# Optimization experiments

Measured on AMD Instinct MI355X. Metric: run time of the kernel, lower is better.

## Reference

```python
import jax, jax.numpy as jnp
import numpy as np
from jax import lax

PAD = 2          # shift_size // 2
SHIFT = 5        # shift_size


def _soft_shift(fp, gw, gb, axis):
    """fp: padded feature map [B,C,Hp,Wp]; gw: [S,C] 1x1-conv weight; gb: [S].
    Gated soft-shift along `axis` (2=H, 3=W), then crop padding."""
    logits = jnp.einsum('bchw,sc->bshw', fp, gw) + gb[None, :, None, None]
    w = jax.nn.softmax(logits, axis=1)  # [B,S,Hp,Wp]
    acc = jnp.zeros_like(fp)
    for i, s in enumerate(range(-PAD, PAD + 1)):
        acc = acc + jnp.roll(fp, s, axis=axis) * w[:, i:i + 1]
    return acc[:, :, PAD:-PAD, PAD:-PAD]


def _dwconv(x, w, b):
    # x: [B,C,H,W], w: [C,1,3,3] depthwise, b: [C]
    y = lax.conv_general_dilated(x, w, window_strides=(1, 1), padding='SAME',
                                 dimension_numbers=('NCHW', 'OIHW', 'NCHW'),
                                 feature_group_count=x.shape[1])
    return y + b[None, :, None, None]


def setup_inputs() -> dict:
    key = jax.random.key(0)
    ks = jax.random.split(key, 12)
    B, H, W = 16, 128, 128
    C, Ch = 96, 384
    x = jax.random.normal(ks[0], (B, H * W, C), dtype=jnp.float32)
    fc1_w = jax.random.normal(ks[1], (C, Ch), dtype=jnp.float32) * 0.02
    fc1_b = jnp.zeros((Ch,), dtype=jnp.float32)
    dw_w = jax.random.normal(ks[2], (Ch, 1, 3, 3), dtype=jnp.float32) * np.sqrt(2.0 / 9.0)
    dw_b = jnp.zeros((Ch,), dtype=jnp.float32)
    fc2_w = jax.random.normal(ks[3], (Ch, C), dtype=jnp.float32) * 0.02
    fc2_b = jnp.zeros((C,), dtype=jnp.float32)
    gh_w = jax.random.normal(ks[4], (SHIFT, C), dtype=jnp.float32) * np.sqrt(2.0 / SHIFT)
    gh_b = jnp.zeros((SHIFT,), dtype=jnp.float32)
    gw_w = jax.random.normal(ks[5], (SHIFT, Ch), dtype=jnp.float32) * np.sqrt(2.0 / SHIFT)
    gw_b = jnp.zeros((SHIFT,), dtype=jnp.float32)
    return {"x": x, "H": H, "W": W,
            "fc1_w": fc1_w, "fc1_b": fc1_b, "dw_w": dw_w, "dw_b": dw_b,
            "fc2_w": fc2_w, "fc2_b": fc2_b,
            "gh_w": gh_w, "gh_b": gh_b, "gw_w": gw_w, "gw_b": gw_b}


def reference(x, H, W, fc1_w, fc1_b, dw_w, dw_b, fc2_w, fc2_b, gh_w, gh_b, gw_w, gw_b):
    B, N, C = x.shape
    # soft-shift along H on input channels
    fmap = jnp.transpose(x, (0, 2, 1)).reshape(B, C, H, W)
    fmap_p = jnp.pad(fmap, ((0, 0), (0, 0), (PAD, PAD), (PAD, PAD)))
    mixed_h = _soft_shift(fmap_p, gh_w, gh_b, axis=2)          # [B,C,H,W]
    tokens = jnp.transpose(mixed_h.reshape(B, C, H * W), (0, 2, 1))
    tokens = tokens @ fc1_w + fc1_b                            # [B,N,Ch]
    Ch = tokens.shape[-1]
    t = jnp.transpose(tokens, (0, 2, 1)).reshape(B, Ch, H, W)
    t = _dwconv(t, dw_w, dw_b)
    tokens = jnp.transpose(t.reshape(B, Ch, H * W), (0, 2, 1))
    tokens = jax.nn.gelu(tokens, approximate=False)
    # soft-shift along W on hidden channels
    fmap2 = jnp.transpose(tokens, (0, 2, 1)).reshape(B, Ch, H, W)
    fmap2_p = jnp.pad(fmap2, ((0, 0), (0, 0), (PAD, PAD), (PAD, PAD)))
    mixed_w = _soft_shift(fmap2_p, gw_w, gw_b, axis=3)         # [B,Ch,H,W]
    tokens2 = jnp.transpose(mixed_w.reshape(B, Ch, H * W), (0, 2, 1))
    return tokens2 @ fc2_w + fc2_b                             # [B,N,C_out]
```

## Files before the change

### kernel.cpp

```cpp
#include <hip/hip_runtime.h>
#include <cstddef>

#define Cc 96
#define CH 384
#define Mtok 262144
#define Mi   16384

typedef unsigned short us8 __attribute__((ext_vector_type(8)));
typedef float f8 __attribute__((ext_vector_type(8)));
typedef short s8v __attribute__((ext_vector_type(8)));
typedef float f4v __attribute__((ext_vector_type(4)));

static __device__ __forceinline__ float b2f(unsigned short s){
  union { unsigned u; float f; } v; v.u = ((unsigned)s) << 16; return v.f;
}
static __device__ __forceinline__ unsigned short f2b(float f){
  union { float f; unsigned u; } v; v.f = f;
  unsigned r = v.u + 0x7fffu + ((v.u >> 16) & 1u);
  return (unsigned short)(r >> 16);
}

__global__ __launch_bounds__(64) void k_wprep(const float* __restrict__ dww,
    float* __restrict__ wt_t){
  int i = blockIdx.x*64 + threadIdx.x;
  if (i < 9*CH){
    int tap = i / CH, c = i - tap*CH;
    wt_t[i] = dww[c*9 + tap];
  }
}

__global__ __launch_bounds__(256) void k_wprep2(const float* __restrict__ fc2w,
    unsigned short* __restrict__ Bp){
  int i = blockIdx.x*256 + threadIdx.x;
  int j = i & 7;
  int t = i >> 3;
  int l = t & 63;
  int u = t >> 6;
  int ks = u % 12, nt = u / 12;
  int k   = ks*32 + (l>>4)*8 + j;
  int col = nt*16 + (l&15);
  Bp[i] = f2b(fc2w[(size_t)k*96 + col]);
}

__global__ __launch_bounds__(256) void k_wprep1(const float* __restrict__ fc1w,
    unsigned short* __restrict__ Bp1){
  int i = blockIdx.x*256 + threadIdx.x;
  int j = i & 7;
  int t = i >> 3;
  int l = t & 63;
  int u = t >> 6;
  int ks = u % 3, nt = u / 3;
  int k   = ks*32 + (l>>4)*8 + j;
  int col = nt*16 + (l&15);
  Bp1[i] = f2b(fc1w[(size_t)k*CH + col]);
}

__global__ __launch_bounds__(320) void k_fc1f(const float* __restrict__ x,
    const float* __restrict__ gh_w, const float* __restrict__ gh_b,
    const unsigned short* __restrict__ Bp1, const float* __restrict__ fc1b,
    unsigned short* __restrict__ hid, int base, int Mloc){
  __shared__ unsigned short A[80][100];
  __shared__ unsigned short Y[80][104];
  __shared__ float wh_s[80][5];
  const int tid = threadIdx.x;
  const int bid = (int)blockIdx.x;
  const int img  = bid >> 8;
  const int rem  = bid & 255;
  const int band = rem >> 5;
  const int colg = rem & 31;
  const int h0 = band*16;
  const int w0 = colg*4;
  const size_t lbase = (size_t)img*16384;

  {
    const int sr = tid>>2, sq = tid&3;
    const int r = sr>>2, cw = sr&3;
    const int h = h0 + r - 2;
    const bool valid = ((unsigned)h < 128u);
    float part[5] = {0.f,0.f,0.f,0.f,0.f};
    if (valid){
      const float* src = &x[((size_t)base + lbase + h*128 + w0 + cw)*Cc + sq*24];
      #pragma unroll
      for (int p=0;p<3;++p){
        float4 v0 = *(const float4*)&src[p*8];
        float4 v1 = *(const float4*)&src[p*8+4];
        us8 ov;
        ov[0]=f2b(v0.x); ov[1]=f2b(v0.y); ov[2]=f2b(v0.z); ov[3]=f2b(v0.w);
        ov[4]=f2b(v1.x); ov[5]=f2b(v1.y); ov[6]=f2b(v1.z); ov[7]=f2b(v1.w);
        *(us8*)&A[sr][sq*24 + p*8] = ov;
        #pragma unroll
        for (int s=0;s<5;++s){
          float4 g0 = *(const float4*)&gh_w[s*Cc + sq*24 + p*8];
          float4 g1 = *(const float4*)&gh_w[s*Cc + sq*24 + p*8 + 4];
          part[s]=fmaf(v0.x,g0.x,part[s]); part[s]=fmaf(v0.y,g0.y,part[s]);
          part[s]=fmaf(v0.z,g0.z,part[s]); part[s]=fmaf(v0.w,g0.w,part[s]);
          part[s]=fmaf(v1.x,g1.x,part[s]); part[s]=fmaf(v1.y,g1.y,part[s]);
          part[s]=fmaf(v1.z,g1.z,part[s]); part[s]=fmaf(v1.w,g1.w,part[s]);
        }
      }
    } else {
      us8 z = {0,0,0,0,0,0,0,0};
      #pragma unroll
      for (int p=0;p<3;++p) *(us8*)&A[sr][sq*24 + p*8] = z;
    }
    #pragma unroll
    for (int s=0;s<5;++s){
      float v = part[s];
      v += __shfl_xor(v, 1, 64);
      v += __shfl_xor(v, 2, 64);
      part[s] = v;
    }
    if (sq==0 && valid){
      float l[5];
      #pragma unroll
      for (int s=0;s<5;++s) l[s] = part[s] + gh_b[s];
      float mx = fmaxf(fmaxf(fmaxf(l[0],l[1]),fmaxf(l[2],l[3])),l[4]);
      float sum=0.f;
      #pragma unroll
      for (int s=0;s<5;++s){ l[s]=__expf(l[s]-mx); sum+=l[s]; }
      float inv=1.f/sum;
      #pragma unroll
      for (int s=0;s<5;++s) wh_s[sr][s] = l[s]*inv;
    }
  }
  __syncthreads();

  const int wv = tid>>6, l = tid&63;
  const int row16 = l&15, g = l>>4;
  const int tl = tid>>2, q = tid&3;
  const int it = (2 + (tl>>2))*4 + (tl&3);
  const int hh = h0 + (tl>>2);
  float swgt[5];
  unsigned short* o = nullptr;
  if (tid < 256){
    #pragma unroll
    for (int i=0;i<5;++i){
      int h2 = hh - (i-2);
      swgt[i] = ((unsigned)h2 < 128u) ? wh_s[it][i] : 0.f;
    }
    o = &hid[(lbase + hh*128 + w0 + (tl&3))*CH];
  }

  #pragma unroll 1
  for (int chunk=0;chunk<4;++chunk){
    f4v acc[6];
    #pragma unroll
    for (int j=0;j<6;++j) acc[j] = (f4v){0.f,0.f,0.f,0.f};
    #pragma unroll
    for (int ks=0;ks<3;++ks){
      s8v a = *(const s8v*)&A[wv*16 + row16][ks*32 + g*8];
      #pragma unroll
      for (int j=0;j<6;++j){
        s8v b = *(const s8v*)&Bp1[((size_t)((chunk*6+j)*3+ks)*64 + l)*8];
        acc[j] = __builtin_amdgcn_mfma_f32_16x16x32_bf16(a, b, acc[j], 0, 0, 0);
      }
    }
    __syncthreads();
    #pragma unroll
    for (int j=0;j<6;++j){
      #pragma unroll
      for (int r=0;r<4;++r){
        Y[wv*16 + g*4 + r][j*16 + row16] = f2b(acc[j][r]);
      }
    }
    __syncthreads();
    if (tid < 256){
      const int c0 = chunk*96 + q*24;
      float acc2[24];
      #pragma unroll
      for (int j=0;j<24;++j) acc2[j] = fc1b[c0+j];
      #pragma unroll
      for (int i=0;i<5;++i){
        if (swgt[i] != 0.f){
          const unsigned short* yr = &Y[it - 4*(i-2)][q*24];
          #pragma unroll
          for (int p=0;p<3;++p){
            us8 v = *(const us8*)&yr[p*8];
            #pragma unroll
            for (int j=0;j<8;++j) acc2[p*8+j] = fmaf(swgt[i], b2f(v[j]), acc2[p*8+j]);
          }
        }
      }
      #pragma unroll
      for (int p=0;p<3;++p){
        us8 ov;
        #pragma unroll
        for (int j=0;j<8;++j) ov[j] = f2b(acc2[p*8+j]);
        *(us8*)&o[c0 + p*8] = ov;
      }
    }
  }
}

__global__ __launch_bounds__(256) void k_dw(const unsigned short* __restrict__ hid,
    const float* __restrict__ wt_t, const float* __restrict__ dwb,
    const float* __restrict__ gww, const float* __restrict__ gwb,
    unsigned short* __restrict__ hid2, float* __restrict__ ww, int Mloc){
  const int tid = threadIdx.x;
  const int m0 = blockIdx.x*64;
  const int p  = tid>>3, cg = tid&7;
  const int m  = m0 + 2*p;
  const int h = (m>>7)&127, w = m&127;
  bool hok[3];
  #pragma unroll
  for (int k=0;k<3;++k) hok[k] = ((unsigned)(h+k-1) < 128u);
  bool c0ok = (w > 0);
  bool c3ok = (w <= 125);

  float part0[5] = {0.f,0.f,0.f,0.f,0.f};
  float part1[5] = {0.f,0.f,0.f,0.f,0.f};
  #pragma unroll 1
  for (int cc=0;cc<6;++cc){
    const int c = cg*8 + cc*64;
    float acc0[8], acc1[8];
    {
      f8 bias = *(const f8*)&dwb[c];
      #pragma unroll
      for (int j=0;j<8;++j){ acc0[j] = bias[j]; acc1[j] = bias[j]; }
    }
    #pragma unroll
    for (int kh=0;kh<3;++kh){
      if (!hok[kh]) continue;
      us8 cv[4];
      {
        const unsigned short* rr = &hid[(size_t)(m + (kh-1)*128)*CH + c];
        us8 z = {0,0,0,0,0,0,0,0};
        cv[0] = c0ok ? *(const us8*)(rr - CH)   : z;
        cv[1] = *(const us8*)rr;
        cv[2] = *(const us8*)(rr + CH);
        cv[3] = c3ok ? *(const us8*)(rr + 2*CH) : z;
      }
      #pragma unroll
      for (int kw=0;kw<3;++kw){
        f8 wf = *(const f8*)&wt_t[(kh*3+kw)*CH + c];
        #pragma unroll
        for (int j=0;j<8;++j){
          acc0[j] = fmaf(b2f(cv[kw  ][j]), wf[j], acc0[j]);
          acc1[j] = fmaf(b2f(cv[kw+1][j]), wf[j], acc1[j]);
        }
      }
    }
    us8 ov0, ov1;
    float g0[8], g1[8];
    #pragma unroll
    for (int j=0;j<8;++j){
      float a0 = acc0[j];
      float t0 = __expf(-a0*(1.5957691216f + 0.0713548996f*a0*a0));
      g0[j] = a0*__builtin_amdgcn_rcpf(1.f + t0);
      ov0[j] = f2b(g0[j]);
      float a1 = acc1[j];
      float t1 = __expf(-a1*(1.5957691216f + 0.0713548996f*a1*a1));
      g1[j] = a1*__builtin_amdgcn_rcpf(1.f + t1);
      ov1[j] = f2b(g1[j]);
    }
    *(us8*)&hid2[(size_t)m*CH + c]     = ov0;
    *(us8*)&hid2[(size_t)(m+1)*CH + c] = ov1;
    #pragma unroll
    for (int s=0;s<5;++s){
      f8 gw = *(const f8*)&gww[s*CH + c];
      #pragma unroll
      for (int j=0;j<8;++j){
        part0[s] = fmaf(g0[j], gw[j], part0[s]);
        part1[s] = fmaf(g1[j], gw[j], part1[s]);
      }
    }
  }
  #pragma unroll
  for (int s=0;s<5;++s){
    float v0 = part0[s];
    v0 += __shfl_xor(v0, 1, 64);
    v0 += __shfl_xor(v0, 2, 64);
    v0 += __shfl_xor(v0, 4, 64);
    part0[s] = v0;
    float v1 = part1[s];
    v1 += __shfl_xor(v1, 1, 64);
    v1 += __shfl_xor(v1, 2, 64);
    v1 += __shfl_xor(v1, 4, 64);
    part1[s] = v1;
  }
  if (cg==0){
    float l0[5], l1[5];
    #pragma unroll
    for (int s=0;s<5;++s){ l0[s] = part0[s] + gwb[s]; l1[s] = part1[s] + gwb[s]; }
    float mx0 = fmaxf(fmaxf(fmaxf(l0[0],l0[1]),fmaxf(l0[2],l0[3])),l0[4]);
    float mx1 = fmaxf(fmaxf(fmaxf(l1[0],l1[1]),fmaxf(l1[2],l1[3])),l1[4]);
    float s0=0.f, s1=0.f;
    #pragma unroll
    for (int s=0;s<5;++s){
      l0[s]=__expf(l0[s]-mx0); s0+=l0[s];
      l1[s]=__expf(l1[s]-mx1); s1+=l1[s];
    }
    float i0 = 1.f/s0, i1 = 1.f/s1;
    #pragma unroll
    for (int s=0;s<5;++s){
      ww[(size_t)s*Mloc + m]     = l0[s]*i0;
      ww[(size_t)s*Mloc + m + 1] = l1[s]*i1;
    }
  }
}

__global__ __launch_bounds__(256) void k_fc2(const unsigned short* __restrict__ hid2,
    const unsigned short* __restrict__ Bp, unsigned short* __restrict__ y,
    int Mloc){
  __shared__ unsigned short As[64][392];
  const int tid = threadIdx.x;
  const int m0 = blockIdx.x*64;
  {
    const int sr = tid>>2, sq = tid&3;
    const unsigned short* src = &hid2[(size_t)(m0+sr)*CH + sq*96];
    #pragma unroll
    for (int cc=0;cc<12;++cc)
      *(us8*)&As[sr][sq*96 + cc*8] = *(const us8*)&src[cc*8];
  }
  __syncthreads();

  const int wv = tid>>6, l = tid&63;
  const int row16 = l&15, g = l>>4;
  f4v acc[6];
  #pragma unroll
  for (int nt=0;nt<6;++nt) acc[nt] = (f4v){0.f,0.f,0.f,0.f};

  #pragma unroll
  for (int ks=0;ks<12;++ks){
    s8v a = *(const s8v*)&As[wv*16 + row16][ks*32 + g*8];
    #pragma unroll
    for (int nt=0;nt<6;++nt){
      s8v b = *(const s8v*)&Bp[((size_t)(nt*12+ks)*64 + l)*8];
      acc[nt] = __builtin_amdgcn_mfma_f32_16x16x32_bf16(a, b, acc[nt], 0, 0, 0);
    }
  }

  #pragma unroll
  for (int nt=0;nt<6;++nt){
    #pragma unroll
    for (int r=0;r<4;++r){
      size_t m = (size_t)(m0 + wv*16 + g*4 + r);
      y[m*96 + nt*16 + row16] = f2b(acc[nt][r]);
    }
  }
}

__global__ __launch_bounds__(256) void k_blend(const unsigned short* __restrict__ y,
    const float* __restrict__ ww, const float* __restrict__ fc2b,
    float* __restrict__ out, int base, int Mloc){
  const int tid = threadIdx.x;
  const int m0 = blockIdx.x*64;
  const int tl = tid>>2, q = tid&3;
  const int ml = m0 + tl;
  const int gm = base + ml;
  const int wp = gm & 127;
  float swgt[5];
  #pragma unroll
  for (int i=0;i<5;++i){
    int w2 = wp - (i-2);
    swgt[i] = ((unsigned)w2 < 128u) ? ww[(size_t)i*Mloc + ml] : 0.f;
  }
  const int c0 = q*24;
  float acc[24];
  #pragma unroll
  for (int j=0;j<24;++j) acc[j] = fc2b[c0+j];
  #pragma unroll
  for (int i=0;i<5;++i){
    if (swgt[i] != 0.f){
      const unsigned short* yr = &y[(size_t)(ml-(i-2))*96 + c0];
      #pragma unroll
      for (int p=0;p<3;++p){
        us8 v = *(const us8*)&yr[p*8];
        #pragma unroll
        for (int j=0;j<8;++j) acc[p*8+j] = fmaf(swgt[i], b2f(v[j]), acc[p*8+j]);
      }
    }
  }
  float* o = &out[(size_t)gm*96 + c0];
  #pragma unroll
  for (int p=0;p<6;++p)
    *(float4*)&o[p*4] = make_float4(acc[p*4],acc[p*4+1],acc[p*4+2],acc[p*4+3]);
}

extern "C" void kernel_launch(void* const* d_in, const int* in_sizes, int n_in,
                              void* d_out, int out_size, void* d_ws, size_t ws_size,
                              hipStream_t stream) {
  const float* x     = (const float*)d_in[0];
  const float* fc1_w = (const float*)d_in[3];
  const float* fc1_b = (const float*)d_in[4];
  const float* dw_w  = (const float*)d_in[5];
  const float* dw_b  = (const float*)d_in[6];
  const float* fc2_w = (const float*)d_in[7];
  const float* fc2_b = (const float*)d_in[8];
  const float* gh_w  = (const float*)d_in[9];
  const float* gh_b  = (const float*)d_in[10];
  const float* gw_w  = (const float*)d_in[11];
  const float* gw_b  = (const float*)d_in[12];
  float* out = (float*)d_out;

  float* wt_t = (float*)d_ws;
  unsigned short* Bp  = (unsigned short*)((char*)d_ws + 13824);
  unsigned short* Bp1 = (unsigned short*)((char*)d_ws + 13824 + 73728);
  char*  wsc  = (char*)d_ws + 13824 + 73728 + 73728;
  size_t ws_rem = (ws_size > 161280) ? ws_size - 161280 : 0;

  k_wprep<<<(9*CH + 63)/64, 64, 0, stream>>>(dw_w, wt_t);
  k_wprep2<<<144, 256, 0, stream>>>(fc2_w, Bp);
  k_wprep1<<<144, 256, 0, stream>>>(fc1_w, Bp1);

  const size_t pi = (size_t)5*Mi*4 + (size_t)Mi*CH*2*2 + (size_t)Mi*96*2;
  int NI = (int)(ws_rem / pi);
  if (NI < 1) NI = 1;
  if (NI > 16) NI = 16;

  for (int b0 = 0; b0 < 16; b0 += NI) {
    int nb = (16 - b0 < NI) ? (16 - b0) : NI;
    int Mloc = nb * Mi;
    int base = b0 * Mi;
    float* ww = (float*)wsc;
    unsigned short* hid  = (unsigned short*)(ww + (size_t)5*Mloc);
    unsigned short* hid2 = hid + (size_t)Mloc*CH;
    unsigned short* yb   = hid2 + (size_t)Mloc*CH;
    k_fc1f<<<Mloc/64, 320, 0, stream>>>(x, gh_w, gh_b, Bp1, fc1_b, hid, base, Mloc);
    k_dw<<<Mloc/64, 256, 0, stream>>>(hid, wt_t, dw_b, gw_w, gw_b, hid2, ww, Mloc);
    k_fc2<<<Mloc/64, 256, 0, stream>>>(hid2, Bp, yb, Mloc);
    k_blend<<<Mloc/64, 256, 0, stream>>>(yb, ww, fc2_b, out, base, Mloc);
  }
}
```

Measured before the change: 490.9 us.

## Fuse fc2 GEMM with W-shift blend using halo rows in LDS

Merges the fc2 MFMA GEMM and the softmax-weighted W-direction blend into one kernel. Each 64-token block also computes 4 halo tokens (80 rows, 320 threads), keeping the fc2 output tile in LDS instead of writing and re-reading an intermediate y buffer. This removes one launch and a global round trip, at the cost of about 25% redundant GEMM rows and more LDS per block. It also swizzles the block index in k_dw to spread neighbouring tiles across groups of workgroups.

```diff
diff --git a/kernel.cpp b/kernel.cpp
--- a/kernel.cpp
+++ b/kernel.cpp
@@ -197,7 +197,10 @@
     const float* __restrict__ gww, const float* __restrict__ gwb,
     unsigned short* __restrict__ hid2, float* __restrict__ ww, int Mloc){
   const int tid = threadIdx.x;
-  const int m0 = blockIdx.x*64;
+  const int nwg = (int)gridDim.x;
+  const int bid = (int)blockIdx.x;
+  const int wg  = (bid & 7)*(nwg >> 3) + (bid >> 3);
+  const int m0 = wg*64;
   const int p  = tid>>3, cg = tid&7;
   const int m  = m0 + 2*p;
   const int h = (m>>7)&127, w = m&127;
@@ -299,82 +302,94 @@
   }
 }
 
-__global__ __launch_bounds__(256) void k_fc2(const unsigned short* __restrict__ hid2,
-    const unsigned short* __restrict__ Bp, unsigned short* __restrict__ y,
-    int Mloc){
-  __shared__ unsigned short As[64][392];
+__global__ __launch_bounds__(320) void k_fc2f(const unsigned short* __restrict__ hid2,
+    const float* __restrict__ ww, const unsigned short* __restrict__ Bp,
+    const float* __restrict__ fc2b, float* __restrict__ out,
+    int base, int Mloc){
+  __shared__ unsigned short A[80][100];
+  __shared__ unsigned short Y[80][104];
   const int tid = threadIdx.x;
-  const int m0 = blockIdx.x*64;
-  {
-    const int sr = tid>>2, sq = tid&3;
-    const unsigned short* src = &hid2[(size_t)(m0+sr)*CH + sq*96];
-    #pragma unroll
-    for (int cc=0;cc<12;++cc)
-      *(us8*)&As[sr][sq*96 + cc*8] = *(const us8*)&src[cc*8];
-  }
-  __syncthreads();
+  const int m0 = (int)blockIdx.x*64;
+  const int w0 = m0 & 127;
+  const int rowbase = m0 - w0;
 
   const int wv = tid>>6, l = tid&63;
   const int row16 = l&15, g = l>>4;
+  const int srow = tid>>2, ssq = tid&3;
+  const int swtok = w0 - 2 + srow;
+  const bool svalid = (srow < 68) && ((unsigned)swtok < 128u);
+  const unsigned short* ssrc = svalid ?
+      &hid2[(size_t)(rowbase + swtok)*CH + ssq*24] : nullptr;
+
   f4v acc[6];
   #pragma unroll
-  for (int nt=0;nt<6;++nt) acc[nt] = (f4v){0.f,0.f,0.f,0.f};
-
-  #pragma unroll
-  for (int ks=0;ks<12;++ks){
-    s8v a = *(const s8v*)&As[wv*16 + row16][ks*32 + g*8];
-    #pragma unroll
-    for (int nt=0;nt<6;++nt){
-      s8v b = *(const s8v*)&Bp[((size_t)(nt*12+ks)*64 + l)*8];
-      acc[nt] = __builtin_amdgcn_mfma_f32_16x16x32_bf16(a, b, acc[nt], 0, 0, 0);
-    }
+  for (int j=0;j<6;++j) acc[j] = (f4v){0.f,0.f,0.f,0.f};
+
+  #pragma unroll 1
+  for (int chunk=0;chunk<4;++chunk){
+    if (svalid){
+      #pragma unroll
+      for (int p=0;p<3;++p)
+        *(us8*)&A[srow][ssq*24 + p*8] = *(const us8*)&ssrc[chunk*96 + p*8];
+    } else {
+      us8 z = {0,0,0,0,0,0,0,0};
+      #pragma unroll
+      for (int p=0;p<3;++p) *(us8*)&A[srow][ssq*24 + p*8] = z;
+    }
+    __syncthreads();
+    #pragma unroll
+    for (int ks=0;ks<3;++ks){
+      s8v a = *(const s8v*)&A[wv*16 + row16][ks*32 + g*8];
+      #pragma unroll
+      for (int nt=0;nt<6;++nt){
+        s8v b = *(const s8v*)&Bp[((size_t)(nt*12 + chunk*3 + ks)*64 + l)*8];
+        acc[nt] = __builtin_amdgcn_mfma_f32_16x16x32_bf16(a, b, acc[nt], 0, 0, 0);
+      }
+    }
+    __syncthreads();
   }
 
   #pragma unroll
   for (int nt=0;nt<6;++nt){
     #pragma unroll
     for (int r=0;r<4;++r){
-      size_t m = (size_t)(m0 + wv*16 + g*4 + r);
-      y[m*96 + nt*16 + row16] = f2b(acc[nt][r]);
-    }
-  }
-}
-
-__global__ __launch_bounds__(256) void k_blend(const unsigned short* __restrict__ y,
-    const float* __restrict__ ww, const float* __restrict__ fc2b,
-    float* __restrict__ out, int base, int Mloc){
-  const int tid = threadIdx.x;
-  const int m0 = blockIdx.x*64;
-  const int tl = tid>>2, q = tid&3;
-  const int ml = m0 + tl;
-  const int gm = base + ml;
-  const int wp = gm & 127;
-  float swgt[5];
-  #pragma unroll
-  for (int i=0;i<5;++i){
-    int w2 = wp - (i-2);
-    swgt[i] = ((unsigned)w2 < 128u) ? ww[(size_t)i*Mloc + ml] : 0.f;
-  }
-  const int c0 = q*24;
-  float acc[24];
-  #pragma unroll
-  for (int j=0;j<24;++j) acc[j] = fc2b[c0+j];
-  #pragma unroll
-  for (int i=0;i<5;++i){
-    if (swgt[i] != 0.f){
-      const unsigned short* yr = &y[(size_t)(ml-(i-2))*96 + c0];
-      #pragma unroll
-      for (int p=0;p<3;++p){
-        us8 v = *(const us8*)&yr[p*8];
+      Y[wv*16 + g*4 + r][nt*16 + row16] = f2b(acc[nt][r]);
+    }
+  }
+  __syncthreads();
+
+  if (tid < 256){
+    const int t = tid>>2, q = tid&3;
+    const int ml = m0 + t;
+    const int gm = base + ml;
+    const int wp = w0 + t;
+    float swgt[5];
+    #pragma unroll
+    for (int i=0;i<5;++i){
+      int w2 = wp - (i-2);
+      swgt[i] = ((unsigned)w2 < 128u) ? ww[(size_t)i*Mloc + ml] : 0.f;
+    }
+    const int c0 = q*24;
+    float acc2[24];
+    #pragma unroll
+    for (int j=0;j<24;++j) acc2[j] = fc2b[c0+j];
+    #pragma unroll
+    for (int i=0;i<5;++i){
+      if (swgt[i] != 0.f){
+        const unsigned short* yr = &Y[(t+2) - (i-2)][c0];
         #pragma unroll
-        for (int j=0;j<8;++j) acc[p*8+j] = fmaf(swgt[i], b2f(v[j]), acc[p*8+j]);
-      }
-    }
-  }
-  float* o = &out[(size_t)gm*96 + c0];
-  #pragma unroll
-  for (int p=0;p<6;++p)
-    *(float4*)&o[p*4] = make_float4(acc[p*4],acc[p*4+1],acc[p*4+2],acc[p*4+3]);
+        for (int p=0;p<3;++p){
+          us8 v = *(const us8*)&yr[p*8];
+          #pragma unroll
+          for (int j=0;j<8;++j) acc2[p*8+j] = fmaf(swgt[i], b2f(v[j]), acc2[p*8+j]);
+        }
+      }
+    }
+    float* o = &out[(size_t)gm*96 + c0];
+    #pragma unroll
+    for (int p=0;p<6;++p)
+      *(float4*)&o[p*4] = make_float4(acc2[p*4],acc2[p*4+1],acc2[p*4+2],acc2[p*4+3]);
+  }
 }
 
 extern "C" void kernel_launch(void* const* d_in, const int* in_sizes, int n_in,
@@ -403,7 +418,7 @@
   k_wprep2<<<144, 256, 0, stream>>>(fc2_w, Bp);
   k_wprep1<<<144, 256, 0, stream>>>(fc1_w, Bp1);
 
-  const size_t pi = (size_t)5*Mi*4 + (size_t)Mi*CH*2*2 + (size_t)Mi*96*2;
+  const size_t pi = (size_t)5*Mi*4 + (size_t)Mi*CH*2*2;
   int NI = (int)(ws_rem / pi);
   if (NI < 1) NI = 1;
   if (NI > 16) NI = 16;
@@ -415,10 +430,8 @@
     float* ww = (float*)wsc;
     unsigned short* hid  = (unsigned short*)(ww + (size_t)5*Mloc);
     unsigned short* hid2 = hid + (size_t)Mloc*CH;
-    unsigned short* yb   = hid2 + (size_t)Mloc*CH;
     k_fc1f<<<Mloc/64, 320, 0, stream>>>(x, gh_w, gh_b, Bp1, fc1_b, hid, base, Mloc);
     k_dw<<<Mloc/64, 256, 0, stream>>>(hid, wt_t, dw_b, gw_w, gw_b, hid2, ww, Mloc);
-    k_fc2<<<Mloc/64, 256, 0, stream>>>(hid2, Bp, yb, Mloc);
-    k_blend<<<Mloc/64, 256, 0, stream>>>(yb, ww, fc2_b, out, base, Mloc);
-  }
-}
+    k_fc2f<<<Mloc/64, 320, 0, stream>>>(hid2, ww, Bp, fc2_b, out, base, Mloc);
+  }
+}
```

New measurement: 497.7 us. About the same (+1.4%).
